# Performance work log

Hardware: AMD Instinct MI355X
Metric: run time of the kernel (lower is better)

The kernel has to match this reference:

```python
import jax, jax.numpy as jnp
import numpy as np

B, L, DX, H = 2, 2048, 1024, 16
DQ = DK = DV = DR = 64


def setup_inputs() -> dict:
    key0 = jax.random.key(0)
    ks = jax.random.split(key0, 14)
    def lin(kw, kb, din, dout):
        s = 1.0 / np.sqrt(din)
        w = jax.random.uniform(kw, (din, dout), jnp.float32, -s, s)
        b = jax.random.uniform(kb, (dout,), jnp.float32, -s, s)
        return w, b
    value = jax.random.normal(ks[0], (B, L, DX), jnp.float32)
    key_t = jax.random.normal(ks[1], (B, L, DX), jnp.float32)
    query = jax.random.normal(ks[2], (B, L, DX), jnp.float32)
    mask = jnp.tril(jnp.ones((L, L), jnp.int32))[None, None]  # [1,1,L,L] causal
    Wq_w, Wq_b = lin(ks[3], ks[4], DX, DQ * H)
    Wk_w, Wk_b = lin(ks[5], ks[6], DX, DK * H)
    Wv_w, Wv_b = lin(ks[7], ks[8], DX, DV * H)
    Wr_w, Wr_b = lin(ks[9], ks[10], DX, DR * H)
    wo_w, wo_b = lin(ks[11], ks[12], DV * H, DX)
    return dict(value=value, key=key_t, query=query, mask=mask,
                Wq_w=Wq_w, Wq_b=Wq_b, Wk_w=Wk_w, Wk_b=Wk_b,
                Wv_w=Wv_w, Wv_b=Wv_b, Wr_w=Wr_w, Wr_b=Wr_b,
                wo_w=wo_w, wo_b=wo_b)


def reference(value, key, query, mask, Wq_w, Wq_b, Wk_w, Wk_b, Wv_w, Wv_b,
              Wr_w, Wr_b, wo_w, wo_b):
    N, Lq, _ = query.shape
    q = (query @ Wq_w + Wq_b).reshape(N, Lq, H, DQ)   # nqhd
    k = (key @ Wk_w + Wk_b).reshape(N, -1, H, DK)     # nkhd
    v = (value @ Wv_w + Wv_b).reshape(N, -1, H, DV)   # nlhd
    r = (query @ Wr_w + Wr_b).reshape(N, Lq, H, DR)   # computed but unused (as in source)
    del r
    scores = jnp.einsum('nqhd,nkhd->nhqk', q, k)      # [N,H,L,L] materialized
    scores = jnp.where(mask == 0, jnp.float32(-1e20), scores)
    scale = jnp.float32(np.sqrt(DX))  # source divides by embedding_size**0.5
    attn = jax.nn.softmax(scores / scale, axis=3)
    out = jnp.einsum('nhql,nlhd->nqhd', attn, v).reshape(N, Lq, H * DV)
    return out @ wo_w + wo_b
```

## Files before the change

kernel.cpp:

```cpp
#include <hip/hip_runtime.h>
#include <hip/hip_bf16.h>
#include <type_traits>

typedef __hip_bfloat16 bf16;
typedef __attribute__((ext_vector_type(4))) float f32x4;
typedef __attribute__((ext_vector_type(8))) short s16x8;

#define DEVINL __device__ __forceinline__

DEVINL s16x8 load16B(const void* p) {
  s16x8 v;
  __builtin_memcpy(&v, __builtin_assume_aligned(p, 16), 16);
  return v;
}
DEVINL void store16B(void* p, s16x8 v) {
  __builtin_memcpy(__builtin_assume_aligned(p, 16), &v, 16);
}
DEVINL s16x8 cvt8(const float* p) {
  f32x4 a, b;
  __builtin_memcpy(&a, __builtin_assume_aligned(p, 16), 16);
  __builtin_memcpy(&b, __builtin_assume_aligned(p + 4, 16), 16);
  union { s16x8 v; bf16 h[8]; } u;
#pragma unroll
  for (int i = 0; i < 4; i++) {
    u.h[i] = __float2bfloat16(a[i]);
    u.h[4 + i] = __float2bfloat16(b[i]);
  }
  return u.v;
}
DEVINL void gload_lds16(const bf16* g, bf16* l) {
  __builtin_amdgcn_global_load_lds(
      (__attribute__((address_space(1))) void*)(void*)const_cast<bf16*>(g),
      (__attribute__((address_space(3))) void*)l, 16, 0, 0);
}

static constexpr int SEQ = 2048;

__global__ __launch_bounds__(256) void k_transpose(
    const float* __restrict__ Wq, const float* __restrict__ Wk,
    const float* __restrict__ Wv, const float* __restrict__ Wo,
    bf16* __restrict__ dst) {
  __shared__ float t[64][65];
  const float* src = blockIdx.z == 0 ? Wq : blockIdx.z == 1 ? Wk
                   : blockIdx.z == 2 ? Wv : Wo;
  bf16* out = dst + (size_t)blockIdx.z * 1024 * 1024;
  const int r0 = blockIdx.y * 64, c0 = blockIdx.x * 64;
#pragma unroll
  for (int i = 0; i < 16; i++) {
    int e = i * 256 + threadIdx.x;
    int r = e >> 6, c = e & 63;
    t[r][c] = src[(size_t)(r0 + r) * 1024 + c0 + c];
  }
  __syncthreads();
#pragma unroll
  for (int i = 0; i < 16; i++) {
    int e = i * 256 + threadIdx.x;
    int r = e >> 6, c = e & 63;
    out[(size_t)(c0 + r) * 1024 + r0 + c] = __float2bfloat16(t[c][r]);
  }
}

template <typename XT>
DEVINL void gemm_core(const XT* __restrict__ X, const bf16* __restrict__ WT,
                      const float* __restrict__ bias, void* __restrict__ dstv,
                      const int mode, const float scale, const int m0,
                      const int n0) {
  __shared__ alignas(16) bf16 As[128 * 32];
  __shared__ alignas(16) bf16 Bs[128 * 32];
  const int tid = threadIdx.x;
  const int w = tid >> 6, lane = tid & 63, lg = lane >> 4, li = lane & 15;
  const int wm = w >> 1, wn = w & 1;

  f32x4 acc[4][4] = {};

  for (int kt = 0; kt < 32; ++kt) {
    const int k0 = kt * 32;
#pragma unroll
    for (int j = 0; j < 2; j++) {
      const int cb = (j * 4 + w) * 64;
      const int c = cb + lane;
      const int r = c >> 2, kk = (c & 3) * 8;
      gload_lds16(WT + (size_t)(n0 + r) * 1024 + k0 + kk, Bs + cb * 8);
      if constexpr (std::is_same_v<XT, bf16>)
        gload_lds16(X + (size_t)(m0 + r) * 1024 + k0 + kk, As + cb * 8);
    }
    if constexpr (std::is_same_v<XT, float>) {
#pragma unroll
      for (int j = 0; j < 2; j++) {
        const int c = j * 256 + tid;
        const int r = c >> 2, kk = (c & 3) * 8;
        s16x8 a = cvt8(X + (size_t)(m0 + r) * 1024 + k0 + kk);
        store16B((char*)As + c * 16, a);
      }
    }
    __syncthreads();
    s16x8 af[4], bfv[4];
#pragma unroll
    for (int i = 0; i < 4; i++)
      af[i] = load16B((char*)As + (wm * 64 + i * 16 + li) * 64 + lg * 16);
#pragma unroll
    for (int j = 0; j < 4; j++)
      bfv[j] = load16B((char*)Bs + (wn * 64 + j * 16 + li) * 64 + lg * 16);
#pragma unroll
    for (int i = 0; i < 4; i++)
#pragma unroll
      for (int j = 0; j < 4; j++)
        acc[i][j] = __builtin_amdgcn_mfma_f32_16x16x32_bf16(af[i], bfv[j],
                                                            acc[i][j], 0, 0, 0);
    __syncthreads();
  }

#pragma unroll
  for (int j = 0; j < 4; j++) {
    const int n = n0 + wn * 64 + j * 16 + li;
    const float bv = bias[n];
#pragma unroll
    for (int i = 0; i < 4; i++) {
      const int mrow = m0 + wm * 64 + i * 16 + lg * 4;
      f32x4 a = acc[i][j];
      if (mode == 2) {
        float* dst = (float*)dstv;
#pragma unroll
        for (int r = 0; r < 4; r++)
          dst[(size_t)(mrow + r) * 1024 + n] = a[r] + bv;
      } else if (mode == 0) {
        bf16* dst = (bf16*)dstv;
#pragma unroll
        for (int r = 0; r < 4; r++) {
          int m = mrow + r;
          size_t idx =
              ((size_t)((m >> 11) * 16 + (n >> 6)) * SEQ + (m & 2047)) * 64 +
              (n & 63);
          dst[idx] = __float2bfloat16((a[r] + bv) * scale);
        }
      } else {
        bf16* dst = (bf16*)dstv;
        size_t base =
            ((size_t)((mrow >> 11) * 16 + (n >> 6)) * 64 + (n & 63)) * SEQ +
            (mrow & 2047);
        bf16 tmp[4];
#pragma unroll
        for (int r = 0; r < 4; r++) tmp[r] = __float2bfloat16(a[r] + bv);
        __builtin_memcpy(__builtin_assume_aligned(dst + base, 8), tmp, 8);
      }
    }
  }
}

__global__ __launch_bounds__(256) void k_gemm_qkv(
    const float* __restrict__ qx, const float* __restrict__ kx,
    const float* __restrict__ vx, const bf16* __restrict__ WTbase,
    const float* __restrict__ qb, const float* __restrict__ kb,
    const float* __restrict__ vb, bf16* __restrict__ qo,
    bf16* __restrict__ ko, bf16* __restrict__ vto) {
  const int z = blockIdx.z;
  const float* X = z == 0 ? qx : z == 1 ? kx : vx;
  const bf16* WT = WTbase + (size_t)z * 1048576;
  const float* bias = z == 0 ? qb : z == 1 ? kb : vb;
  void* dst = z == 0 ? (void*)qo : z == 1 ? (void*)ko : (void*)vto;
  gemm_core<float>(X, WT, bias, dst, z == 2 ? 1 : 0, z == 0 ? 0.03125f : 1.0f,
                   blockIdx.x * 128, blockIdx.y * 128);
}

__global__ __launch_bounds__(256) void k_gemm_out(
    const bf16* __restrict__ X, const bf16* __restrict__ WT,
    const float* __restrict__ bias, float* __restrict__ out) {
  gemm_core<bf16>(X, WT, bias, out, 2, 1.0f, blockIdx.x * 128,
                  blockIdx.y * 128);
}

__global__ __launch_bounds__(256) void k_attn(
    const bf16* __restrict__ qb, const bf16* __restrict__ kb,
    const bf16* __restrict__ vtb, bf16* __restrict__ attn) {
  __shared__ alignas(16) bf16 Ks[2][64 * 64];
  __shared__ alignas(16) bf16 Vts[2][64 * 64];
  __shared__ alignas(16) bf16 Ps[4][16 * 72];
  const int tid = threadIdx.x;
  const int w = tid >> 6, lane = tid & 63, lg = lane >> 4, li = lane & 15;
  const int bh = blockIdx.x;
  const int qblk = 31 - blockIdx.y;
  const int qrow = qblk * 64 + w * 16;
  const bf16* qh = qb + (size_t)bh * SEQ * 64;
  const bf16* kh = kb + (size_t)bh * SEQ * 64;
  const bf16* vth = vtb + (size_t)bh * 64 * SEQ;

  s16x8 aq[2];
#pragma unroll
  for (int c = 0; c < 2; c++)
    aq[c] = load16B(qh + (size_t)(qrow + li) * 64 + c * 32 + lg * 8);

  f32x4 o[4] = {};
  float m_run = -1e38f;
  float l_run = 0.f;

  const int c0s = tid, c1s = 256 + tid;
  const int by0 = (c0s * 16) ^ (((c0s >> 3) & 7) << 4);
  const int by1 = (c1s * 16) ^ (((c1s >> 3) & 7) << 4);
  const int d0 = c0s >> 3, kk0 = (c0s & 7) * 8;
  const int d1 = c1s >> 3, kk1 = (c1s & 7) * 8;

  s16x8 rk[2], rv[2];
  rk[0] = load16B(kh + (size_t)c0s * 8);
  rk[1] = load16B(kh + (size_t)c1s * 8);
  rv[0] = load16B(vth + (size_t)d0 * SEQ + kk0);
  rv[1] = load16B(vth + (size_t)d1 * SEQ + kk1);
  store16B((char*)Ks[0] + by0, rk[0]);
  store16B((char*)Ks[0] + by1, rk[1]);
  store16B((char*)Vts[0] + by0, rv[0]);
  store16B((char*)Vts[0] + by1, rv[1]);
  if (qblk >= 1) {
    rk[0] = load16B(kh + (size_t)64 * 64 + c0s * 8);
    rk[1] = load16B(kh + (size_t)64 * 64 + c1s * 8);
    rv[0] = load16B(vth + (size_t)d0 * SEQ + 64 + kk0);
    rv[1] = load16B(vth + (size_t)d1 * SEQ + 64 + kk1);
  }
  __syncthreads();

  for (int kbk = 0; kbk <= qblk; ++kbk) {
    const int cur = kbk & 1;
    if (kbk < qblk) {
      store16B((char*)Ks[cur ^ 1] + by0, rk[0]);
      store16B((char*)Ks[cur ^ 1] + by1, rk[1]);
      store16B((char*)Vts[cur ^ 1] + by0, rv[0]);
      store16B((char*)Vts[cur ^ 1] + by1, rv[1]);
      if (kbk + 2 <= qblk) {
        const int kn = (kbk + 2) * 64;
        rk[0] = load16B(kh + (size_t)kn * 64 + c0s * 8);
        rk[1] = load16B(kh + (size_t)kn * 64 + c1s * 8);
        rv[0] = load16B(vth + (size_t)d0 * SEQ + kn + kk0);
        rv[1] = load16B(vth + (size_t)d1 * SEQ + kn + kk1);
      }
    }

    f32x4 s[4];
    __builtin_amdgcn_s_setprio(1);
#pragma unroll
    for (int t = 0; t < 4; t++) {
      f32x4 z = {};
#pragma unroll
      for (int c = 0; c < 2; c++) {
        int row = t * 16 + li;
        s16x8 ak = load16B((char*)Ks[cur] +
                           ((row * 128 + c * 64 + lg * 16) ^ ((row & 7) << 4)));
        z = __builtin_amdgcn_mfma_f32_16x16x32_bf16(ak, aq[c], z, 0, 0, 0);
      }
      s[t] = z;
    }
    __builtin_amdgcn_s_setprio(0);

    if (kbk == qblk) {
      const int kb0 = kbk * 64 + lg * 4;
      const int qg = qrow + li;
#pragma unroll
      for (int t = 0; t < 4; t++)
#pragma unroll
        for (int r = 0; r < 4; r++)
          if (kb0 + t * 16 + r > qg) s[t][r] = -1e30f;
    }

    f32x4 mm = s[0];
#pragma unroll
    for (int t = 1; t < 4; t++)
#pragma unroll
      for (int r = 0; r < 4; r++) mm[r] = fmaxf(mm[r], s[t][r]);
    float mr = fmaxf(fmaxf(mm[0], mm[1]), fmaxf(mm[2], mm[3]));
    mr = fmaxf(mr, __shfl_xor(mr, 16));
    mr = fmaxf(mr, __shfl_xor(mr, 32));
    const float mn = fmaxf(m_run, mr);

    float p[4][4];
    float sum = 0.f;
#pragma unroll
    for (int t = 0; t < 4; t++)
#pragma unroll
      for (int r = 0; r < 4; r++) {
        float pv = __expf(s[t][r] - mn);
        p[t][r] = pv;
        sum += pv;
      }
    sum += __shfl_xor(sum, 16);
    sum += __shfl_xor(sum, 32);
    const float cr = __expf(m_run - mn);
    l_run = l_run * cr + sum;
    m_run = mn;

#pragma unroll
    for (int t = 0; t < 4; t++) {
      bf16 tmp[4];
#pragma unroll
      for (int r = 0; r < 4; r++) tmp[r] = __float2bfloat16(p[t][r]);
      __builtin_memcpy(
          __builtin_assume_aligned(&Ps[w][li * 72 + t * 16 + lg * 4], 8), tmp,
          8);
    }

    const int sb = (lane & 48);
    float crr[4];
#pragma unroll
    for (int r = 0; r < 4; r++) crr[r] = __shfl(cr, sb + (sb >> 2) + r);
#pragma unroll
    for (int t = 0; t < 4; t++)
#pragma unroll
      for (int r = 0; r < 4; r++) o[t][r] *= crr[r];

    s16x8 ap[2];
#pragma unroll
    for (int c = 0; c < 2; c++)
      ap[c] = load16B(&Ps[w][li * 72 + c * 32 + lg * 8]);

    __builtin_amdgcn_s_setprio(1);
#pragma unroll
    for (int t = 0; t < 4; t++) {
#pragma unroll
      for (int c = 0; c < 2; c++) {
        int row = t * 16 + li;
        s16x8 bv = load16B((char*)Vts[cur] +
                           ((row * 128 + c * 64 + lg * 16) ^ ((row & 7) << 4)));
        o[t] = __builtin_amdgcn_mfma_f32_16x16x32_bf16(ap[c], bv, o[t], 0, 0, 0);
      }
    }
    __builtin_amdgcn_s_setprio(0);
    __syncthreads();
  }

  const int b = bh >> 4, h = bh & 15;
  const float inv = 1.0f / l_run;
  const int sb = (lane & 48);
  float invr[4];
#pragma unroll
  for (int r = 0; r < 4; r++) invr[r] = __shfl(inv, sb + (sb >> 2) + r);
#pragma unroll
  for (int r = 0; r < 4; r++)
#pragma unroll
    for (int t = 0; t < 4; t++) {
      size_t idx = (size_t)(b * SEQ + qrow + lg * 4 + r) * 1024 + h * 64 +
                   t * 16 + li;
      attn[idx] = __float2bfloat16(o[t][r] * invr[r]);
    }
}

extern "C" void kernel_launch(void* const* d_in, const int* in_sizes, int n_in,
                              void* d_out, int out_size, void* d_ws,
                              size_t ws_size, hipStream_t stream) {
  (void)in_sizes; (void)n_in; (void)out_size; (void)ws_size;
  const float* value = (const float*)d_in[0];
  const float* key   = (const float*)d_in[1];
  const float* query = (const float*)d_in[2];
  const float* Wq_w = (const float*)d_in[4];
  const float* Wq_b = (const float*)d_in[5];
  const float* Wk_w = (const float*)d_in[6];
  const float* Wk_b = (const float*)d_in[7];
  const float* Wv_w = (const float*)d_in[8];
  const float* Wv_b = (const float*)d_in[9];
  const float* wo_w = (const float*)d_in[12];
  const float* wo_b = (const float*)d_in[13];

  bf16* ws = (bf16*)d_ws;
  const size_t MM = 1048576;
  bf16* WT   = ws;
  bf16* qbuf = ws + 4 * MM;
  bf16* kbuf = ws + 8 * MM;
  bf16* vtbf = ws + 12 * MM;
  bf16* abuf = ws + 16 * MM;

  k_transpose<<<dim3(16, 16, 4), 256, 0, stream>>>(Wq_w, Wk_w, Wv_w, wo_w, WT);
  k_gemm_qkv<<<dim3(32, 8, 3), 256, 0, stream>>>(
      query, key, value, WT, Wq_b, Wk_b, Wv_b, qbuf, kbuf, vtbf);
  k_attn<<<dim3(32, 32), 256, 0, stream>>>(qbuf, kbuf, vtbf, abuf);
  k_gemm_out<<<dim3(32, 8), 256, 0, stream>>>(abuf, WT + 3 * MM, wo_b,
                                              (float*)d_out);
}
```

Baseline: 119.7 us.

## Double-buffer GEMM LDS tiles and prefetch fp32 activations into registers

The projection GEMM core now uses two LDS buffers for the A and B tiles. The next k-tile's async global-to-LDS loads are issued while the MFMAs run on the current tile, and the per-iteration barriers drop from two to one. For fp32 inputs, the tile two steps ahead is preloaded into registers and converted to bf16 when stored. This aims to hide global load latency behind compute, at the cost of twice the LDS and extra registers, which may lower occupancy.

```diff
diff --git a/kernel.cpp b/kernel.cpp
--- a/kernel.cpp
+++ b/kernel.cpp
@@ -16,10 +16,11 @@
 DEVINL void store16B(void* p, s16x8 v) {
   __builtin_memcpy(__builtin_assume_aligned(p, 16), &v, 16);
 }
-DEVINL s16x8 cvt8(const float* p) {
-  f32x4 a, b;
+DEVINL void loadA8(const float* p, f32x4& a, f32x4& b) {
   __builtin_memcpy(&a, __builtin_assume_aligned(p, 16), 16);
   __builtin_memcpy(&b, __builtin_assume_aligned(p + 4, 16), 16);
+}
+DEVINL s16x8 pack8(f32x4 a, f32x4 b) {
   union { s16x8 v; bf16 h[8]; } u;
 #pragma unroll
   for (int i = 0; i < 4; i++) {
@@ -27,6 +28,11 @@
     u.h[4 + i] = __float2bfloat16(b[i]);
   }
   return u.v;
+}
+DEVINL s16x8 cvt8(const float* p) {
+  f32x4 a, b;
+  loadA8(p, a, b);
+  return pack8(a, b);
 }
 DEVINL void gload_lds16(const bf16* g, bf16* l) {
   __builtin_amdgcn_global_load_lds(
@@ -65,42 +71,68 @@
                       const float* __restrict__ bias, void* __restrict__ dstv,
                       const int mode, const float scale, const int m0,
                       const int n0) {
-  __shared__ alignas(16) bf16 As[128 * 32];
-  __shared__ alignas(16) bf16 Bs[128 * 32];
+  __shared__ alignas(16) bf16 As[2][128 * 32];
+  __shared__ alignas(16) bf16 Bs[2][128 * 32];
   const int tid = threadIdx.x;
   const int w = tid >> 6, lane = tid & 63, lg = lane >> 4, li = lane & 15;
   const int wm = w >> 1, wn = w & 1;
 
   f32x4 acc[4][4] = {};
+  f32x4 ar[4];
+
+  const int ca0 = tid, ca1 = 256 + tid;
+  const int ra0 = ca0 >> 2, ka0 = (ca0 & 3) * 8;
+  const int ra1 = ca1 >> 2, ka1 = (ca1 & 3) * 8;
+
+#pragma unroll
+  for (int j = 0; j < 2; j++) {
+    const int cb = (j * 4 + w) * 64;
+    const int c = cb + lane;
+    const int r = c >> 2, kk = (c & 3) * 8;
+    gload_lds16(WT + (size_t)(n0 + r) * 1024 + kk, Bs[0] + cb * 8);
+    if constexpr (std::is_same_v<XT, bf16>)
+      gload_lds16(X + (size_t)(m0 + r) * 1024 + kk, As[0] + cb * 8);
+  }
+  if constexpr (std::is_same_v<XT, float>) {
+    store16B((char*)As[0] + ca0 * 16, cvt8(X + (size_t)(m0 + ra0) * 1024 + ka0));
+    store16B((char*)As[0] + ca1 * 16, cvt8(X + (size_t)(m0 + ra1) * 1024 + ka1));
+    loadA8(X + (size_t)(m0 + ra0) * 1024 + 32 + ka0, ar[0], ar[1]);
+    loadA8(X + (size_t)(m0 + ra1) * 1024 + 32 + ka1, ar[2], ar[3]);
+  }
+  __syncthreads();
 
   for (int kt = 0; kt < 32; ++kt) {
-    const int k0 = kt * 32;
-#pragma unroll
-    for (int j = 0; j < 2; j++) {
-      const int cb = (j * 4 + w) * 64;
-      const int c = cb + lane;
-      const int r = c >> 2, kk = (c & 3) * 8;
-      gload_lds16(WT + (size_t)(n0 + r) * 1024 + k0 + kk, Bs + cb * 8);
-      if constexpr (std::is_same_v<XT, bf16>)
-        gload_lds16(X + (size_t)(m0 + r) * 1024 + k0 + kk, As + cb * 8);
-    }
-    if constexpr (std::is_same_v<XT, float>) {
+    const int cur = kt & 1;
+    if (kt < 31) {
+      const int k1 = (kt + 1) * 32;
 #pragma unroll
       for (int j = 0; j < 2; j++) {
-        const int c = j * 256 + tid;
+        const int cb = (j * 4 + w) * 64;
+        const int c = cb + lane;
         const int r = c >> 2, kk = (c & 3) * 8;
-        s16x8 a = cvt8(X + (size_t)(m0 + r) * 1024 + k0 + kk);
-        store16B((char*)As + c * 16, a);
-      }
-    }
-    __syncthreads();
+        gload_lds16(WT + (size_t)(n0 + r) * 1024 + k1 + kk,
+                    Bs[cur ^ 1] + cb * 8);
+        if constexpr (std::is_same_v<XT, bf16>)
+          gload_lds16(X + (size_t)(m0 + r) * 1024 + k1 + kk,
+                      As[cur ^ 1] + cb * 8);
+      }
+      if constexpr (std::is_same_v<XT, float>) {
+        store16B((char*)As[cur ^ 1] + ca0 * 16, pack8(ar[0], ar[1]));
+        store16B((char*)As[cur ^ 1] + ca1 * 16, pack8(ar[2], ar[3]));
+        if (kt < 30) {
+          const int k2 = (kt + 2) * 32;
+          loadA8(X + (size_t)(m0 + ra0) * 1024 + k2 + ka0, ar[0], ar[1]);
+          loadA8(X + (size_t)(m0 + ra1) * 1024 + k2 + ka1, ar[2], ar[3]);
+        }
+      }
+    }
     s16x8 af[4], bfv[4];
 #pragma unroll
     for (int i = 0; i < 4; i++)
-      af[i] = load16B((char*)As + (wm * 64 + i * 16 + li) * 64 + lg * 16);
+      af[i] = load16B((char*)As[cur] + (wm * 64 + i * 16 + li) * 64 + lg * 16);
 #pragma unroll
     for (int j = 0; j < 4; j++)
-      bfv[j] = load16B((char*)Bs + (wn * 64 + j * 16 + li) * 64 + lg * 16);
+      bfv[j] = load16B((char*)Bs[cur] + (wn * 64 + j * 16 + li) * 64 + lg * 16);
 #pragma unroll
     for (int i = 0; i < 4; i++)
 #pragma unroll
```

Result: slower. 128.3 us (+7.2%).
